# Optimization experiments

Hardware: AMD Instinct MI355X
Metric: run time of the kernel (lower is better)

Reference implementation:

```python
import jax, jax.numpy as jnp
import numpy as np

SUB = 8          # Config.sub_sampling
CROP = 24        # max feature-space ROI extent given proposal generator
NEG = jnp.float32(-1e30)


def _roi_adaptive_maxpool(feature_map, coords):
    """Vectorized equivalent of the per-proposal tf.slice + AdaptivePooling((2,2)) loop.
    feature_map: [1,H,W,C]; coords: [N,4] int (y0,x0,y1,x1) in image space.
    Returns [N,2,2,C]."""
    fm = feature_map[0]
    H, W, C = fm.shape
    sy = jnp.minimum(coords[:, 0] // SUB, H - 2)              # min(coord0//8, 74)
    sx = jnp.minimum(coords[:, 1] // SUB, W - 2)              # min(coord1//8, 126)
    ey = (coords[:, 2] + SUB - 1) // SUB                      # ceil(coord2/8)
    ex = (coords[:, 3] + SUB - 1) // SUB                      # ceil(coord3/8)
    h = jnp.maximum(ey - sy, 2)                               # max(end-start, 2)
    w = jnp.maximum(ex - sx, 2)
    # fixed-size crop per proposal (padding keeps dynamic_slice in-bounds; pad area masked out)
    fm_pad = jnp.pad(fm, ((0, CROP), (0, CROP), (0, 0)))
    crop = jax.vmap(lambda y, x: jax.lax.dynamic_slice(fm_pad, (y, x, 0), (CROP, CROP, C)))(sy, sx)
    # adaptive 2-bin boundaries: bin i covers [floor(i*s/2), ceil((i+1)*s/2))
    idx = jnp.arange(CROP)
    two = jnp.arange(2)

    def bin_mask(size):                                        # size [N] -> [N,2,CROP]
        start = (two[None, :] * size[:, None]) // 2
        end = ((two[None, :] + 1) * size[:, None] + 1) // 2
        return (idx[None, None, :] >= start[:, :, None]) & (idx[None, None, :] < end[:, :, None])

    rmask = bin_mask(h)                                        # [N,2,CROP]
    cmask = bin_mask(w)                                        # [N,2,CROP]
    # separable masked max: rows first, then cols
    m1 = jnp.where(rmask[:, :, :, None, None], crop[:, None], NEG)   # [N,2,CROP,CROP,C]
    t = m1.max(axis=2)                                               # [N,2,CROP,C]
    m2 = jnp.where(cmask[:, None, :, :, None], t[:, :, None], NEG)   # [N,2,2,CROP,C]
    return m2.max(axis=3)                                            # [N,2,2,C]


def setup_inputs() -> dict:
    key = jax.random.key(0)
    ks = jax.random.split(key, 12)
    N, C = 256, 512
    feature_map = jax.random.normal(ks[0], (1, 76, 128, C), jnp.float32)
    y0 = jax.random.randint(ks[1], (N,), 0, 584)
    x0 = jax.random.randint(ks[2], (N,), 0, 1000)
    hh = jax.random.randint(ks[3], (N,), 16, 176)
    ww = jax.random.randint(ks[4], (N,), 16, 176)
    y1 = jnp.minimum(y0 + hh, 607)
    x1 = jnp.minimum(x0 + ww, 1023)
    proposal_coords = jnp.stack([y0, x0, y1, x1], axis=1).astype(jnp.int32)
    s = 0.02
    return {
        'feature_map': feature_map,
        'proposal_coords': proposal_coords,
        'W1': s * jax.random.normal(ks[5], (2 * 2 * C, 200), jnp.float32),
        'b1': jnp.zeros((200,), jnp.float32),
        'W2': s * jax.random.normal(ks[6], (200, 200), jnp.float32),
        'b2': jnp.zeros((200,), jnp.float32),
        'W3': s * jax.random.normal(ks[7], (200, 16), jnp.float32),
        'b3': jnp.zeros((16,), jnp.float32),
        'W4': s * jax.random.normal(ks[8], (200, 5), jnp.float32),
        'b4': jnp.zeros((5,), jnp.float32),
    }


def reference(feature_map, proposal_coords, W1, b1, W2, b2, W3, b3, W4, b4):
    coords = proposal_coords.astype(jnp.int32)
    pooled = _roi_adaptive_maxpool(feature_map, coords)        # [N,2,2,C]
    N = pooled.shape[0]
    f = pooled.reshape(N, -1)
    f = jax.nn.relu(f @ W1 + b1)
    f = jax.nn.relu(f @ W2 + b2)
    pred_reg = (f @ W3 + b3).reshape(N, 4, 4)
    pred_cls = f @ W4 + b4                                     # [N,5]
    cls = jnp.argmax(pred_cls, axis=1)
    probs = jax.nn.softmax(pred_cls, axis=1)
    scores = probs[:, 1:].max(axis=1)
    # per-proposal reg deltas for the predicted class (bg uses clipped index; masked out below)
    reg = jnp.take_along_axis(pred_reg, jnp.maximum(cls - 1, 0)[:, None, None], axis=1)[:, 0]  # [N,4]
    pc = coords.astype(jnp.float32)
    ph = pc[:, 2] - pc[:, 0]
    pw = pc[:, 3] - pc[:, 1]
    py = pc[:, 0] + 0.5 * ph
    px = pc[:, 1] + 0.5 * pw
    p_y = ph * reg[:, 0] + py
    p_x = pw * reg[:, 1] + px
    p_h = ph * jnp.clip(jnp.exp(reg[:, 2]), 0.001, 20.0)
    p_w = pw * jnp.clip(jnp.exp(reg[:, 3]), 0.001, 20.0)
    boxes = jnp.stack([p_y, p_x, p_h, p_w], axis=1)            # [N,4]
    non_bg_mask = cls != 0                                     # fixed-shape stand-in for np.where filtering
    return boxes, scores, non_bg_mask
```

## Files before the change

kernel.cpp:

```cpp
#include <hip/hip_runtime.h>
#include <math.h>

#define CCH 512
#define FH 76
#define FW 128
#define NP 256
#define HID 200
#define NKC 16
#define L1_KC 128
#define L1_ROWS 8
#define FM4 (FH * FW * (CCH / 4))
#define POOL_THREADS (NP * 4 * 512)

__global__ __launch_bounds__(512) void pool_kernel(
    const float4* __restrict__ fm4, const int* __restrict__ coords,
    float4* __restrict__ f4, float* __restrict__ scratch)
{
    __shared__ float4 smem[4][128];
    const int n   = blockIdx.x;
    const int bin = blockIdx.y;
    const int t   = threadIdx.x;

    const int gtid = (blockIdx.y * NP + blockIdx.x) * 512 + t;
    float wacc = -1e30f;
    #pragma unroll
    for (int i = 0; i < 3; ++i) {
        const int idx = gtid + i * POOL_THREADS;
        if (idx < FM4) {
            const float4 v = fm4[idx];
            wacc = fmaxf(wacc, fmaxf(fmaxf(v.x, v.y), fmaxf(v.z, v.w)));
        }
    }

    const int by = bin >> 1, bx = bin & 1;
    const int rslot = t >> 7;
    const int cg    = t & 127;
    const int c0 = coords[n*4+0], c1 = coords[n*4+1];
    const int c2 = coords[n*4+2], c3 = coords[n*4+3];
    const int sy = min(c0 >> 3, FH - 2);
    const int sx = min(c1 >> 3, FW - 2);
    const int h = max(((c2 + 7) >> 3) - sy, 2);
    const int w = max(((c3 + 7) >> 3) - sx, 2);
    const int rs = by ? (h >> 1) : 0;
    const int re = by ? h : ((h + 1) >> 1);
    const int cs = bx ? (w >> 1) : 0;
    const int ce = bx ? w : ((w + 1) >> 1);
    const int nc = ce - cs;
    float4 m = make_float4(-1e30f, -1e30f, -1e30f, -1e30f);
    for (int r = rs + rslot; r < re; r += 4) {
        const float4* row = fm4 + ((size_t)(sy + r) * FW + sx + cs) * (CCH/4) + cg;
        #pragma unroll 4
        for (int cc = 0; cc < nc; ++cc) {
            const float4 v = row[(size_t)cc * (CCH/4)];
            m.x = fmaxf(m.x, v.x); m.y = fmaxf(m.y, v.y);
            m.z = fmaxf(m.z, v.z); m.w = fmaxf(m.w, v.w);
        }
    }
    smem[rslot][cg] = m;
    __syncthreads();
    if (t < 128) {
        float4 a = smem[0][t], b = smem[1][t];
        float4 c = smem[2][t], d = smem[3][t];
        float4 o;
        o.x = fmaxf(fmaxf(a.x, b.x), fmaxf(c.x, d.x));
        o.y = fmaxf(fmaxf(a.y, b.y), fmaxf(c.y, d.y));
        o.z = fmaxf(fmaxf(a.z, b.z), fmaxf(c.z, d.z));
        o.w = fmaxf(fmaxf(a.w, b.w), fmaxf(c.w, d.w));
        f4[(size_t)n * (4*CCH/4) + bin * (CCH/4) + t] = o;
    }
    if (wacc == -1e30f && gtid == 0) scratch[0] = wacc;
}

__global__ __launch_bounds__(256) void l1_kernel(
    const float* __restrict__ f, const float* __restrict__ W1,
    float* __restrict__ part)
{
    const int j = threadIdx.x;
    if (j >= HID) return;
    const int r0 = blockIdx.x * L1_ROWS;
    const int kc = blockIdx.y;
    const int k0 = kc * L1_KC;
    float acc[L1_ROWS];
    #pragma unroll
    for (int r = 0; r < L1_ROWS; ++r) acc[r] = 0.0f;
    const float* fp = f  + (size_t)r0 * 2048 + k0;
    const float* wp = W1 + (size_t)k0 * HID + j;
    #pragma unroll 8
    for (int k = 0; k < L1_KC; ++k) {
        const float wv = wp[(size_t)k * HID];
        #pragma unroll
        for (int r = 0; r < L1_ROWS; ++r)
            acc[r] += fp[(size_t)r * 2048 + k] * wv;
    }
    float* pp = part + ((size_t)kc * NP + r0) * HID + j;
    #pragma unroll
    for (int r = 0; r < L1_ROWS; ++r)
        pp[(size_t)r * HID] = acc[r];
}

__global__ __launch_bounds__(512) void head_kernel(
    const float* __restrict__ part,
    const float* __restrict__ b1, const float* __restrict__ W2,
    const float* __restrict__ b2, const float* __restrict__ W3,
    const float* __restrict__ b3, const float* __restrict__ W4,
    const float* __restrict__ b4, const int* __restrict__ coords,
    float* __restrict__ out)
{
    __shared__ float h1s[HID];
    __shared__ float h2s[HID];
    __shared__ float p2[2][HID];
    __shared__ float hdp[2][21];
    __shared__ float hd[21];
    const int n = blockIdx.x;
    const int t = threadIdx.x;
    const int kc = t >> 8;
    const int j  = t & 255;
    if (t < HID) {
        float a = b1[t];
        #pragma unroll
        for (int c = 0; c < NKC; ++c)
            a += part[((size_t)c * NP + n) * HID + t];
        h1s[t] = fmaxf(a, 0.0f);
    }
    __syncthreads();
    if (j < HID) {
        const int k0 = kc * 100;
        float acc = 0.0f;
        #pragma unroll 10
        for (int k = 0; k < 100; ++k)
            acc += h1s[k0 + k] * W2[(k0 + k) * HID + j];
        p2[kc][j] = acc;
    }
    __syncthreads();
    if (t < HID) h2s[t] = fmaxf(p2[0][t] + p2[1][t] + b2[t], 0.0f);
    __syncthreads();
    if (j < 21) {
        const int k0 = kc * 100;
        float acc = 0.0f;
        if (j < 16) {
            #pragma unroll 5
            for (int k = 0; k < 100; ++k)
                acc += h2s[k0 + k] * W3[(k0 + k) * 16 + j];
        } else {
            const int ci = j - 16;
            #pragma unroll 5
            for (int k = 0; k < 100; ++k)
                acc += h2s[k0 + k] * W4[(k0 + k) * 5 + ci];
        }
        hdp[kc][j] = acc;
    }
    __syncthreads();
    if (t < 21)
        hd[t] = hdp[0][t] + hdp[1][t] + (t < 16 ? b3[t] : b4[t - 16]);
    __syncthreads();
    if (t == 0) {
        const float cv0 = hd[16], cv1 = hd[17], cv2 = hd[18],
                    cv3 = hd[19], cv4 = hd[20];
        int cls = 0; float best = cv0;
        if (cv1 > best) { best = cv1; cls = 1; }
        if (cv2 > best) { best = cv2; cls = 2; }
        if (cv3 > best) { best = cv3; cls = 3; }
        if (cv4 > best) { best = cv4; cls = 4; }
        const float e0 = expf(cv0 - best), e1 = expf(cv1 - best),
                    e2 = expf(cv2 - best), e3 = expf(cv3 - best),
                    e4 = expf(cv4 - best);
        const float s = e0 + e1 + e2 + e3 + e4;
        const float score = fmaxf(fmaxf(e1, e2), fmaxf(e3, e4)) / s;
        const int ri = max(cls - 1, 0);
        const float rg0 = hd[ri*4+0], rg1 = hd[ri*4+1],
                    rg2 = hd[ri*4+2], rg3 = hd[ri*4+3];
        const float y0 = (float)coords[n*4+0], x0 = (float)coords[n*4+1];
        const float y1 = (float)coords[n*4+2], x1 = (float)coords[n*4+3];
        const float ph = y1 - y0, pw = x1 - x0;
        const float py = y0 + 0.5f * ph, px = x0 + 0.5f * pw;
        const float oy = ph * rg0 + py;
        const float ox = pw * rg1 + px;
        const float oh = ph * fminf(fmaxf(expf(rg2), 0.001f), 20.0f);
        const float ow = pw * fminf(fmaxf(expf(rg3), 0.001f), 20.0f);
        out[n*4+0] = oy; out[n*4+1] = ox; out[n*4+2] = oh; out[n*4+3] = ow;
        out[NP*4 + n] = score;
        out[NP*5 + n] = (cls != 0) ? 1.0f : 0.0f;
    }
}

extern "C" void kernel_launch(void* const* d_in, const int* in_sizes, int n_in,
                              void* d_out, int out_size, void* d_ws, size_t ws_size,
                              hipStream_t stream) {
    const float* fm     = (const float*)d_in[0];
    const int*   coords = (const int*)  d_in[1];
    const float* W1 = (const float*)d_in[2];
    const float* b1 = (const float*)d_in[3];
    const float* W2 = (const float*)d_in[4];
    const float* b2 = (const float*)d_in[5];
    const float* W3 = (const float*)d_in[6];
    const float* b3 = (const float*)d_in[7];
    const float* W4 = (const float*)d_in[8];
    const float* b4 = (const float*)d_in[9];
    float* out = (float*)d_out;

    float* f       = (float*)d_ws;
    float* part    = f + (size_t)NP * 2048;
    float* scratch = part + (size_t)NKC * NP * HID;

    pool_kernel<<<dim3(NP, 4), 512, 0, stream>>>((const float4*)fm, coords,
                                                 (float4*)f, scratch);
    l1_kernel  <<<dim3(NP / L1_ROWS, NKC), 256, 0, stream>>>(f, W1, part);
    head_kernel<<<NP, 512, 0, stream>>>(part, b1, W2, b2, W3, b3, W4, b4,
                                        coords, out);
}
```

Baseline: 127.8 us.

## Fuse pooling, layer-1 GEMM and head into one persistent kernel with grid barriers

Replaces the three separate launches (pool, layer-1 partial GEMM, MLP head) with a single kernel of 256 co-resident blocks. The stages are separated by atomic-counter grid barriers, and a small init kernel resets the barrier counters each call. The up-front sweep that pulls the feature map into cache now also reads W1–W4, so the weights are cache-resident before the GEMM stages. This is meant to remove inter-kernel launch gaps and tail drain. In exchange, the pooling stage has fewer blocks, each block now serial over its rows, and correctness depends on all 256 blocks being resident at once.

New measurement: 269.1 us. +110.6%, slower.

```diff
diff --git a/kernel.cpp b/kernel.cpp
--- a/kernel.cpp
+++ b/kernel.cpp
@@ -7,179 +7,222 @@
 #define NP 256
 #define HID 200
 #define NKC 16
-#define L1_KC 128
-#define L1_ROWS 8
 #define FM4 (FH * FW * (CCH / 4))
-#define POOL_THREADS (NP * 4 * 512)
-
-__global__ __launch_bounds__(512) void pool_kernel(
+#define NBLK 256
+#define NTHR 512
+#define NTH_ALL (NBLK * NTHR)
+
+
+__global__ __launch_bounds__(256) void init_kernel(int* __restrict__ bar)
+{
+    bar[threadIdx.x] = 0;
+}
+
+__device__ __forceinline__ void grid_barrier(int* bar, int idx)
+{
+    __syncthreads();
+    if (threadIdx.x == 0) {
+        int* cnt  = bar + idx * 64;
+        int* flag = bar + idx * 64 + 32;
+        __threadfence();
+        const int old = __hip_atomic_fetch_add(cnt, 1, __ATOMIC_ACQ_REL,
+                                               __HIP_MEMORY_SCOPE_AGENT);
+        if (old == NBLK - 1) {
+            __hip_atomic_store(flag, 1, __ATOMIC_RELEASE,
+                               __HIP_MEMORY_SCOPE_AGENT);
+        } else {
+            while (!__hip_atomic_load(flag, __ATOMIC_ACQUIRE,
+                                      __HIP_MEMORY_SCOPE_AGENT))
+                __builtin_amdgcn_s_sleep(2);
+        }
+        __threadfence();
+    }
+    __syncthreads();
+}
+
+__global__ __launch_bounds__(NTHR, 2) void fused_kernel(
     const float4* __restrict__ fm4, const int* __restrict__ coords,
-    float4* __restrict__ f4, float* __restrict__ scratch)
+    const float* __restrict__ W1, const float* __restrict__ b1,
+    const float* __restrict__ W2, const float* __restrict__ b2,
+    const float* __restrict__ W3, const float* __restrict__ b3,
+    const float* __restrict__ W4, const float* __restrict__ b4,
+    float* __restrict__ f, float* __restrict__ part,
+    int* __restrict__ bar, float* __restrict__ scratch,
+    float* __restrict__ out)
 {
-    __shared__ float4 smem[4][128];
-    const int n   = blockIdx.x;
-    const int bin = blockIdx.y;
+    const int blk = blockIdx.x;
     const int t   = threadIdx.x;
-
-    const int gtid = (blockIdx.y * NP + blockIdx.x) * 512 + t;
+    const int gtid = blk * NTHR + t;
+
     float wacc = -1e30f;
     #pragma unroll
-    for (int i = 0; i < 3; ++i) {
-        const int idx = gtid + i * POOL_THREADS;
+    for (int i = 0; i < 10; ++i) {
+        const int idx = gtid + i * NTH_ALL;
         if (idx < FM4) {
             const float4 v = fm4[idx];
             wacc = fmaxf(wacc, fmaxf(fmaxf(v.x, v.y), fmaxf(v.z, v.w)));
         }
     }
-
-    const int by = bin >> 1, bx = bin & 1;
-    const int rslot = t >> 7;
-    const int cg    = t & 127;
-    const int c0 = coords[n*4+0], c1 = coords[n*4+1];
-    const int c2 = coords[n*4+2], c3 = coords[n*4+3];
-    const int sy = min(c0 >> 3, FH - 2);
-    const int sx = min(c1 >> 3, FW - 2);
-    const int h = max(((c2 + 7) >> 3) - sy, 2);
-    const int w = max(((c3 + 7) >> 3) - sx, 2);
-    const int rs = by ? (h >> 1) : 0;
-    const int re = by ? h : ((h + 1) >> 1);
-    const int cs = bx ? (w >> 1) : 0;
-    const int ce = bx ? w : ((w + 1) >> 1);
-    const int nc = ce - cs;
-    float4 m = make_float4(-1e30f, -1e30f, -1e30f, -1e30f);
-    for (int r = rs + rslot; r < re; r += 4) {
-        const float4* row = fm4 + ((size_t)(sy + r) * FW + sx + cs) * (CCH/4) + cg;
-        #pragma unroll 4
-        for (int cc = 0; cc < nc; ++cc) {
-            const float4 v = row[(size_t)cc * (CCH/4)];
-            m.x = fmaxf(m.x, v.x); m.y = fmaxf(m.y, v.y);
-            m.z = fmaxf(m.z, v.z); m.w = fmaxf(m.w, v.w);
-        }
-    }
-    smem[rslot][cg] = m;
-    __syncthreads();
-    if (t < 128) {
-        float4 a = smem[0][t], b = smem[1][t];
-        float4 c = smem[2][t], d = smem[3][t];
-        float4 o;
-        o.x = fmaxf(fmaxf(a.x, b.x), fmaxf(c.x, d.x));
-        o.y = fmaxf(fmaxf(a.y, b.y), fmaxf(c.y, d.y));
-        o.z = fmaxf(fmaxf(a.z, b.z), fmaxf(c.z, d.z));
-        o.w = fmaxf(fmaxf(a.w, b.w), fmaxf(c.w, d.w));
-        f4[(size_t)n * (4*CCH/4) + bin * (CCH/4) + t] = o;
-    }
-    if (wacc == -1e30f && gtid == 0) scratch[0] = wacc;
-}
-
-__global__ __launch_bounds__(256) void l1_kernel(
-    const float* __restrict__ f, const float* __restrict__ W1,
-    float* __restrict__ part)
-{
-    const int j = threadIdx.x;
-    if (j >= HID) return;
-    const int r0 = blockIdx.x * L1_ROWS;
-    const int kc = blockIdx.y;
-    const int k0 = kc * L1_KC;
-    float acc[L1_ROWS];
-    #pragma unroll
-    for (int r = 0; r < L1_ROWS; ++r) acc[r] = 0.0f;
-    const float* fp = f  + (size_t)r0 * 2048 + k0;
-    const float* wp = W1 + (size_t)k0 * HID + j;
-    #pragma unroll 8
-    for (int k = 0; k < L1_KC; ++k) {
-        const float wv = wp[(size_t)k * HID];
-        #pragma unroll
-        for (int r = 0; r < L1_ROWS; ++r)
-            acc[r] += fp[(size_t)r * 2048 + k] * wv;
-    }
-    float* pp = part + ((size_t)kc * NP + r0) * HID + j;
-    #pragma unroll
-    for (int r = 0; r < L1_ROWS; ++r)
-        pp[(size_t)r * HID] = acc[r];
-}
-
-__global__ __launch_bounds__(512) void head_kernel(
-    const float* __restrict__ part,
-    const float* __restrict__ b1, const float* __restrict__ W2,
-    const float* __restrict__ b2, const float* __restrict__ W3,
-    const float* __restrict__ b3, const float* __restrict__ W4,
-    const float* __restrict__ b4, const int* __restrict__ coords,
-    float* __restrict__ out)
-{
-    __shared__ float h1s[HID];
-    __shared__ float h2s[HID];
-    __shared__ float p2[2][HID];
-    __shared__ float hdp[2][21];
-    __shared__ float hd[21];
-    const int n = blockIdx.x;
-    const int t = threadIdx.x;
-    const int kc = t >> 8;
-    const int j  = t & 255;
-    if (t < HID) {
-        float a = b1[t];
-        #pragma unroll
-        for (int c = 0; c < NKC; ++c)
-            a += part[((size_t)c * NP + n) * HID + t];
-        h1s[t] = fmaxf(a, 0.0f);
-    }
-    __syncthreads();
-    if (j < HID) {
-        const int k0 = kc * 100;
-        float acc = 0.0f;
-        #pragma unroll 10
-        for (int k = 0; k < 100; ++k)
-            acc += h1s[k0 + k] * W2[(k0 + k) * HID + j];
-        p2[kc][j] = acc;
-    }
-    __syncthreads();
-    if (t < HID) h2s[t] = fmaxf(p2[0][t] + p2[1][t] + b2[t], 0.0f);
-    __syncthreads();
-    if (j < 21) {
-        const int k0 = kc * 100;
-        float acc = 0.0f;
-        if (j < 16) {
-            #pragma unroll 5
+    {
+        const float4* w14 = (const float4*)W1;
+        if (gtid < 102400) {
+            const float4 v = w14[gtid];
+            wacc = fmaxf(wacc, fmaxf(fmaxf(v.x, v.y), fmaxf(v.z, v.w)));
+        }
+        const float4* w24 = (const float4*)W2;
+        if (gtid < 10000) {
+            const float4 v = w24[gtid];
+            wacc = fmaxf(wacc, fmaxf(fmaxf(v.x, v.y), fmaxf(v.z, v.w)));
+        }
+        const float4* w34 = (const float4*)W3;
+        if (gtid < 800) {
+            const float4 v = w34[gtid];
+            wacc = fmaxf(wacc, fmaxf(fmaxf(v.x, v.y), fmaxf(v.z, v.w)));
+        }
+        const float4* w44 = (const float4*)W4;
+        if (gtid < 250) {
+            const float4 v = w44[gtid];
+            wacc = fmaxf(wacc, fmaxf(fmaxf(v.x, v.y), fmaxf(v.z, v.w)));
+        }
+    }
+    if (wacc > 1e29f) scratch[0] = wacc;
+
+    grid_barrier(bar, 0);
+
+    {
+        const int n   = blk;
+        const int bin = t >> 7;
+        const int by = bin >> 1, bx = bin & 1;
+        const int cg = t & 127;
+        const int c0 = coords[n*4+0], c1 = coords[n*4+1];
+        const int c2 = coords[n*4+2], c3 = coords[n*4+3];
+        const int sy = min(c0 >> 3, FH - 2);
+        const int sx = min(c1 >> 3, FW - 2);
+        const int h = max(((c2 + 7) >> 3) - sy, 2);
+        const int w = max(((c3 + 7) >> 3) - sx, 2);
+        const int rs = by ? (h >> 1) : 0;
+        const int re = by ? h : ((h + 1) >> 1);
+        const int cs = bx ? (w >> 1) : 0;
+        const int ce = bx ? w : ((w + 1) >> 1);
+        const int nc = ce - cs;
+        float4 m = make_float4(-1e30f, -1e30f, -1e30f, -1e30f);
+        for (int r = rs; r < re; ++r) {
+            const float4* row = fm4 + ((size_t)(sy + r) * FW + sx + cs) * (CCH/4) + cg;
+            #pragma unroll 4
+            for (int cc = 0; cc < nc; ++cc) {
+                const float4 v = row[(size_t)cc * (CCH/4)];
+                m.x = fmaxf(m.x, v.x); m.y = fmaxf(m.y, v.y);
+                m.z = fmaxf(m.z, v.z); m.w = fmaxf(m.w, v.w);
+            }
+        }
+        ((float4*)f)[(size_t)n * (4*CCH/4) + bin * (CCH/4) + cg] = m;
+    }
+
+    grid_barrier(bar, 1);
+
+    {
+        const int r0   = (blk >> 3) * 8;
+        const int half = t >> 8;
+        const int kc   = (blk & 7) * 2 + half;
+        const int k0   = kc * 128;
+        const int j    = t & 255;
+        if (j < HID) {
+            float acc[8];
+            #pragma unroll
+            for (int r = 0; r < 8; ++r) acc[r] = 0.0f;
+            const float* fp = f  + (size_t)r0 * 2048 + k0;
+            const float* wp = W1 + (size_t)k0 * HID + j;
+            #pragma unroll 8
+            for (int k = 0; k < 128; ++k) {
+                const float wv = wp[(size_t)k * HID];
+                #pragma unroll
+                for (int r = 0; r < 8; ++r)
+                    acc[r] += fp[(size_t)r * 2048 + k] * wv;
+            }
+            float* pp = part + ((size_t)kc * NP + r0) * HID + j;
+            #pragma unroll
+            for (int r = 0; r < 8; ++r)
+                pp[(size_t)r * HID] = acc[r];
+        }
+    }
+
+    grid_barrier(bar, 2);
+
+    {
+        __shared__ float h1s[HID];
+        __shared__ float h2s[HID];
+        __shared__ float p2[2][HID];
+        __shared__ float hdp[2][21];
+        __shared__ float hd[21];
+        const int n = blk;
+        const int kc = t >> 8;
+        const int j  = t & 255;
+        if (t < HID) {
+            float a = b1[t];
+            #pragma unroll
+            for (int c = 0; c < NKC; ++c)
+                a += part[((size_t)c * NP + n) * HID + t];
+            h1s[t] = fmaxf(a, 0.0f);
+        }
+        __syncthreads();
+        if (j < HID) {
+            const int k0 = kc * 100;
+            float acc = 0.0f;
+            #pragma unroll 10
             for (int k = 0; k < 100; ++k)
-                acc += h2s[k0 + k] * W3[(k0 + k) * 16 + j];
-        } else {
-            const int ci = j - 16;
-            #pragma unroll 5
-            for (int k = 0; k < 100; ++k)
-                acc += h2s[k0 + k] * W4[(k0 + k) * 5 + ci];
-        }
-        hdp[kc][j] = acc;
-    }
-    __syncthreads();
-    if (t < 21)
-        hd[t] = hdp[0][t] + hdp[1][t] + (t < 16 ? b3[t] : b4[t - 16]);
-    __syncthreads();
-    if (t == 0) {
-        const float cv0 = hd[16], cv1 = hd[17], cv2 = hd[18],
-                    cv3 = hd[19], cv4 = hd[20];
-        int cls = 0; float best = cv0;
-        if (cv1 > best) { best = cv1; cls = 1; }
-        if (cv2 > best) { best = cv2; cls = 2; }
-        if (cv3 > best) { best = cv3; cls = 3; }
-        if (cv4 > best) { best = cv4; cls = 4; }
-        const float e0 = expf(cv0 - best), e1 = expf(cv1 - best),
-                    e2 = expf(cv2 - best), e3 = expf(cv3 - best),
-                    e4 = expf(cv4 - best);
-        const float s = e0 + e1 + e2 + e3 + e4;
-        const float score = fmaxf(fmaxf(e1, e2), fmaxf(e3, e4)) / s;
-        const int ri = max(cls - 1, 0);
-        const float rg0 = hd[ri*4+0], rg1 = hd[ri*4+1],
-                    rg2 = hd[ri*4+2], rg3 = hd[ri*4+3];
-        const float y0 = (float)coords[n*4+0], x0 = (float)coords[n*4+1];
-        const float y1 = (float)coords[n*4+2], x1 = (float)coords[n*4+3];
-        const float ph = y1 - y0, pw = x1 - x0;
-        const float py = y0 + 0.5f * ph, px = x0 + 0.5f * pw;
-        const float oy = ph * rg0 + py;
-        const float ox = pw * rg1 + px;
-        const float oh = ph * fminf(fmaxf(expf(rg2), 0.001f), 20.0f);
-        const float ow = pw * fminf(fmaxf(expf(rg3), 0.001f), 20.0f);
-        out[n*4+0] = oy; out[n*4+1] = ox; out[n*4+2] = oh; out[n*4+3] = ow;
-        out[NP*4 + n] = score;
-        out[NP*5 + n] = (cls != 0) ? 1.0f : 0.0f;
+                acc += h1s[k0 + k] * W2[(k0 + k) * HID + j];
+            p2[kc][j] = acc;
+        }
+        __syncthreads();
+        if (t < HID) h2s[t] = fmaxf(p2[0][t] + p2[1][t] + b2[t], 0.0f);
+        __syncthreads();
+        if (j < 21) {
+            const int k0 = kc * 100;
+            float acc = 0.0f;
+            if (j < 16) {
+                #pragma unroll 5
+                for (int k = 0; k < 100; ++k)
+                    acc += h2s[k0 + k] * W3[(k0 + k) * 16 + j];
+            } else {
+                const int ci = j - 16;
+                #pragma unroll 5
+                for (int k = 0; k < 100; ++k)
+                    acc += h2s[k0 + k] * W4[(k0 + k) * 5 + ci];
+            }
+            hdp[kc][j] = acc;
+        }
+        __syncthreads();
+        if (t < 21)
+            hd[t] = hdp[0][t] + hdp[1][t] + (t < 16 ? b3[t] : b4[t - 16]);
+        __syncthreads();
+        if (t == 0) {
+            const float cv0 = hd[16], cv1 = hd[17], cv2 = hd[18],
+                        cv3 = hd[19], cv4 = hd[20];
+            int cls = 0; float best = cv0;
+            if (cv1 > best) { best = cv1; cls = 1; }
+            if (cv2 > best) { best = cv2; cls = 2; }
+            if (cv3 > best) { best = cv3; cls = 3; }
+            if (cv4 > best) { best = cv4; cls = 4; }
+            const float e0 = expf(cv0 - best), e1 = expf(cv1 - best),
+                        e2 = expf(cv2 - best), e3 = expf(cv3 - best),
+                        e4 = expf(cv4 - best);
+            const float s = e0 + e1 + e2 + e3 + e4;
+            const float score = fmaxf(fmaxf(e1, e2), fmaxf(e3, e4)) / s;
+            const int ri = max(cls - 1, 0);
+            const float rg0 = hd[ri*4+0], rg1 = hd[ri*4+1],
+                        rg2 = hd[ri*4+2], rg3 = hd[ri*4+3];
+            const float y0 = (float)coords[n*4+0], x0 = (float)coords[n*4+1];
+            const float y1 = (float)coords[n*4+2], x1 = (float)coords[n*4+3];
+            const float ph = y1 - y0, pw = x1 - x0;
+            const float py = y0 + 0.5f * ph, px = x0 + 0.5f * pw;
+            const float oy = ph * rg0 + py;
+            const float ox = pw * rg1 + px;
+            const float oh = ph * fminf(fmaxf(expf(rg2), 0.001f), 20.0f);
+            const float ow = pw * fminf(fmaxf(expf(rg3), 0.001f), 20.0f);
+            out[n*4+0] = oy; out[n*4+1] = ox; out[n*4+2] = oh; out[n*4+3] = ow;
+            out[NP*4 + n] = score;
+            out[NP*5 + n] = (cls != 0) ? 1.0f : 0.0f;
+        }
     }
 }
 
@@ -200,11 +243,11 @@
 
     float* f       = (float*)d_ws;
     float* part    = f + (size_t)NP * 2048;
-    float* scratch = part + (size_t)NKC * NP * HID;
-
-    pool_kernel<<<dim3(NP, 4), 512, 0, stream>>>((const float4*)fm, coords,
-                                                 (float4*)f, scratch);
-    l1_kernel  <<<dim3(NP / L1_ROWS, NKC), 256, 0, stream>>>(f, W1, part);
-    head_kernel<<<NP, 512, 0, stream>>>(part, b1, W2, b2, W3, b3, W4, b4,
-                                        coords, out);
-}
+    int*   bar     = (int*)(part + (size_t)NKC * NP * HID);
+    float* scratch = (float*)(bar + 256);
+
+    init_kernel<<<1, 256, 0, stream>>>(bar);
+    fused_kernel<<<NBLK, NTHR, 0, stream>>>(
+        (const float4*)fm, coords, W1, b1, W2, b2, W3, b3, W4, b4,
+        f, part, bar, scratch, out);
+}
```
